# Optimization experiments

Measured on AMD Instinct MI355X. Metric: run time of the kernel, lower is better.

The kernel has to match this reference:

```python
import jax, jax.numpy as jnp
import numpy as np

B, H, L, D, LBL = 512, 64, 528, 32, 10
NI = 64          # number of interval breakpoints
W = 128          # vf MLP width
N_STEPS = 256    # fixed Tsit5 steps over [t0, t1]

# Tsit5 Butcher tableau
C2, C3, C4, C5, C6 = 0.161, 0.327, 0.9, 0.9800255409045097, 1.0
A21 = 0.161
A31, A32 = -0.008480655492356989, 0.335480655492357
A41, A42, A43 = 2.8971530571054935, -6.359448489975075, 4.3622954328695815
A51, A52, A53, A54 = 5.325864828439257, -11.748883564062828, 7.4955393428898365, -0.09249506636175525
A61, A62, A63, A64, A65 = 5.86145544294642, -12.92096931784711, 8.159367898576159, -0.071584973281401, -0.028269050394068383
B1, B2, B3, B4, B5, B6 = 0.09646076681806523, 0.01, 0.4798896504144996, 1.379008574103742, -3.290069515436081, 2.324710524099774


def _linear_init(k, out_dim, in_dim):
    lim = 1.0 / np.sqrt(in_dim)
    kw, kb = jax.random.split(k)
    w = jax.random.uniform(kw, (out_dim, in_dim), jnp.float32, -lim, lim)
    b = jax.random.uniform(kb, (out_dim,), jnp.float32, -lim, lim)
    return w, b


def setup_inputs() -> dict:
    key = jax.random.key(0)
    ks = jax.random.split(key, 8)
    ts = jnp.linspace(0.0, 1.0, 129, dtype=jnp.float32)
    logsig = 0.1 * jax.random.normal(ks[0], (B, NI + 1, L + 1), jnp.float32)
    x0 = jax.random.normal(ks[1], (B, D), jnp.float32)
    intervals = jnp.linspace(0.0, 1.0, NI, dtype=jnp.float32)
    vf_w0, vf_b0 = _linear_init(ks[2], W, H)
    vf_w1, vf_b1 = _linear_init(ks[3], W, W)
    vf_w2, vf_b2 = _linear_init(ks[4], W, W)
    vf_w3, vf_b3 = _linear_init(ks[5], H * L, W)
    l1_w, l1_b = _linear_init(ks[6], H, D)
    l2_w, l2_b = _linear_init(ks[7], LBL, H)
    return dict(ts=ts, logsig=logsig, x0=x0, intervals=intervals,
                vf_w0=vf_w0, vf_b0=vf_b0, vf_w1=vf_w1, vf_b1=vf_b1,
                vf_w2=vf_w2, vf_b2=vf_b2, vf_w3=vf_w3, vf_b3=vf_b3,
                l1_w=l1_w, l1_b=l1_b, l2_w=l2_w, l2_b=l2_b)


def reference(ts, logsig, x0, intervals,
              vf_w0, vf_b0, vf_w1, vf_b1, vf_w2, vf_b2, vf_w3, vf_b3,
              l1_w, l1_b, l2_w, l2_b):
    Bn = x0.shape[0]
    Hn = l1_w.shape[0]
    Ln = vf_b3.shape[0] // Hn

    def vf(y):  # y: (B, H) -> (B, H, L)
        h = jax.nn.silu(y @ vf_w0.T + vf_b0)
        h = jax.nn.silu(h @ vf_w1.T + vf_b1)
        h = jax.nn.silu(h @ vf_w2.T + vf_b2)
        out = jnp.tanh(h @ vf_w3.T + vf_b3)
        return out.reshape(Bn, Hn, Ln)

    def func(t, y):
        idx = jnp.searchsorted(intervals, t)
        sig = logsig[:, idx, 1:]          # (B, L)
        return jnp.einsum('bhl,bl->bh', vf(y), sig)

    t0, t1 = ts[0], ts[-1]
    dt = (t1 - t0) / N_STEPS

    def step(y, i):
        t = t0 + i * dt
        k1 = func(t, y)
        k2 = func(t + C2 * dt, y + dt * (A21 * k1))
        k3 = func(t + C3 * dt, y + dt * (A31 * k1 + A32 * k2))
        k4 = func(t + C4 * dt, y + dt * (A41 * k1 + A42 * k2 + A43 * k3))
        k5 = func(t + C5 * dt, y + dt * (A51 * k1 + A52 * k2 + A53 * k3 + A54 * k4))
        k6 = func(t + C6 * dt, y + dt * (A61 * k1 + A62 * k2 + A63 * k3 + A64 * k4 + A65 * k5))
        y_new = y + dt * (B1 * k1 + B2 * k2 + B3 * k3 + B4 * k4 + B5 * k5 + B6 * k6)
        return y_new, None

    y0 = x0 @ l1_w.T + l1_b
    yT, _ = jax.lax.scan(step, y0, jnp.arange(N_STEPS, dtype=jnp.float32))
    return jax.nn.softmax(yT @ l2_w.T + l2_b, axis=-1)
```

## Files before the change

kernel.cpp:

```cpp
#include <hip/hip_runtime.h>
#include <stdint.h>

#define NBLK 256
#define NTHR 512

typedef __attribute__((ext_vector_type(8))) short short8;
typedef __attribute__((ext_vector_type(4))) float float4_;

#define WS_BAR  0
#define WS_HDNF 16384
#define WS_KF   (16384 + 131072)
#define WS_SGT  (16384 + 131072 + 262144)

#define LOADC(p)    __hip_atomic_load((p),  __ATOMIC_RELAXED, __HIP_MEMORY_SCOPE_SYSTEM)
#define STOREC(p,v) __hip_atomic_store((p), (v), __ATOMIC_RELAXED, __HIP_MEMORY_SCOPE_SYSTEM)

__device__ __forceinline__ unsigned short f2bf(float x) {
  union { float f; unsigned u; } v; v.f = x;
  return (unsigned short)((v.u + 0x7fffu + ((v.u >> 16) & 1u)) >> 16);
}
__device__ __forceinline__ float fast_exp(float x) {
  return __builtin_amdgcn_exp2f(x * 1.4426950408889634f);
}
__device__ __forceinline__ float fast_tanh(float x) {
  float e = __builtin_amdgcn_exp2f(x * 2.8853900817779268f);
  return fmaf(-2.0f, __builtin_amdgcn_rcpf(e + 1.0f), 1.0f);
}
__device__ __forceinline__ float fast_silu(float x) {
  float e = fast_exp(-x);
  return x * __builtin_amdgcn_rcpf(1.0f + e);
}

__device__ __forceinline__ void gridbar(unsigned* bar, int g, unsigned bn) {
  __syncthreads();
  if (threadIdx.x == 0) {
    unsigned* leaf = bar + 32 * (g & 7);
    unsigned* root = bar + 32 * 8;
    unsigned* gen  = bar + 32 * (9 + (g & 7));
    unsigned a = __hip_atomic_fetch_add(leaf, 1u, __ATOMIC_RELAXED, __HIP_MEMORY_SCOPE_SYSTEM);
    if (a == 32u * bn - 1u) {
      unsigned r = __hip_atomic_fetch_add(root, 1u, __ATOMIC_RELAXED, __HIP_MEMORY_SCOPE_SYSTEM);
      if (r == 8u * bn - 1u) {
        #pragma unroll
        for (int j = 0; j < 8; ++j) STOREC(bar + 32 * (9 + j), bn);
      }
    }
    while (LOADC(gen) < bn) __builtin_amdgcn_s_sleep(1);
  }
  __syncthreads();
}

__device__ __forceinline__ void rgbar(unsigned* bar, int h, int Rg, unsigned bn) {
  __syncthreads();
  if (threadIdx.x == 0) {
    unsigned* base = bar + 32 * (32 + Rg * 16);
    unsigned* leaf = base + 32 * (h & 7);
    unsigned* root = base + 32 * 8;
    unsigned* gen  = base + 32 * 9;
    unsigned a = __hip_atomic_fetch_add(leaf, 1u, __ATOMIC_RELAXED, __HIP_MEMORY_SCOPE_SYSTEM);
    if (a == 8u * bn - 1u) {
      unsigned r = __hip_atomic_fetch_add(root, 1u, __ATOMIC_RELAXED, __HIP_MEMORY_SCOPE_SYSTEM);
      if (r == 8u * bn - 1u) STOREC(gen, bn);
    }
    while (LOADC(gen) < bn) __builtin_amdgcn_s_sleep(1);
  }
  __syncthreads();
}

template<int SIN>
__device__ __forceinline__ void rk_stage(
    int stepi, int sg, int g, int h, int Rg, int R,
    float (&kh)[6], float& y, float t0v, float dtv,
    unsigned char* ws, unsigned* BAR, unsigned& gseq, unsigned& rseq, int& last_idx,
    const float* logsig, const float* w0, const float* b0,
    const float* w1, const float* b1, const float* w2, const float* b2,
    unsigned short* w3lds, float* b3lds, float* intv,
    float (*yst)[64], float (*hb1)[128], float (*hb2)[128],
    unsigned short (*hdnS)[128], int* sidxp, int* sidxnp) {
  const int tid = threadIdx.x;
  const int lane = tid & 63, wv = tid >> 6;
  const int col = lane & 15, qd = lane >> 4;
  unsigned* HDNF = (unsigned*)(ws + WS_HDNF);
  float* KF  = (float*)(ws + WS_KF);
  float* SGT = (float*)(ws + WS_SGT);

  if (sg > 0 && tid < 128) {
    const float* KFr = KF + ((sg & 1) ^ 1) * 32768;
    constexpr int pi = (SIN == 0) ? 5 : SIN - 1;
    kh[pi] = LOADC(&KFr[(size_t)(2 * g + (tid >> 6)) * 64 + (tid & 63)]);
  }
  if (tid < 128) {
    float ystv;
    if constexpr (SIN == 0) {
      if (sg > 0) {
        y += dtv * (0.09646076681806523f * kh[0] + 0.01f * kh[1]
                  + 0.4798896504144996f * kh[2] + 1.379008574103742f * kh[3]
                  - 3.290069515436081f * kh[4] + 2.324710524099774f * kh[5]);
      }
      ystv = y;
    } else if constexpr (SIN == 1) {
      ystv = y + dtv * (0.161f * kh[0]);
    } else if constexpr (SIN == 2) {
      ystv = y + dtv * (-0.008480655492356989f * kh[0] + 0.335480655492357f * kh[1]);
    } else if constexpr (SIN == 3) {
      ystv = y + dtv * (2.8971530571054935f * kh[0] - 6.359448489975075f * kh[1]
                      + 4.3622954328695815f * kh[2]);
    } else if constexpr (SIN == 4) {
      ystv = y + dtv * (5.325864828439257f * kh[0] - 11.748883564062828f * kh[1]
                      + 7.4955393428898365f * kh[2] - 0.09249506636175525f * kh[3]);
    } else {
      ystv = y + dtv * (5.86145544294642f * kh[0] - 12.92096931784711f * kh[1]
                      + 8.159367898576159f * kh[2] - 0.071584973281401f * kh[3]
                      - 0.028269050394068383f * kh[4]);
    }
    yst[tid >> 6][tid & 63] = ystv;
  }
  {
    float tb = __fadd_rn(t0v, __fmul_rn((float)stepi, dtv));
    float t_cur, t_nxt;
    if constexpr (SIN == 0) t_cur = tb;
    else {
      constexpr float cS = (SIN == 1) ? 0.161f : (SIN == 2) ? 0.327f : (SIN == 3) ? 0.9f
                         : (SIN == 4) ? 0.9800255409045097f : 1.0f;
      t_cur = __fadd_rn(tb, __fmul_rn(cS, dtv));
    }
    if constexpr (SIN == 5) t_nxt = __fadd_rn(t0v, __fmul_rn((float)(stepi + 1), dtv));
    else {
      constexpr float cN = (SIN == 0) ? 0.161f : (SIN == 1) ? 0.327f : (SIN == 2) ? 0.9f
                         : (SIN == 3) ? 0.9800255409045097f : 1.0f;
      t_nxt = __fadd_rn(tb, __fmul_rn(cN, dtv));
    }
    if (tid < 64) {
      unsigned long long m1 = __ballot(intv[tid] < t_cur);
      unsigned long long m2 = __ballot(intv[tid] < t_nxt);
      if (tid == 0) { *sidxp = (int)__popcll(m1); *sidxnp = (int)__popcll(m2); }
    }
  }
  __syncthreads();
  const int idx = *sidxp, idxn = *sidxnp;
  const bool rebuild = (idx != last_idx);
  const bool rebuild_next = (idxn != idx);
  last_idx = idx;
  if (rebuild && g < 33) {
    const int l0t = g * 16;
    const int part = tid & 3;
    #pragma unroll 1
    for (int bi = 0; bi < 4; ++bi) {
      const int b = bi * 128 + (tid >> 2);
      const float* srow = logsig + ((size_t)b * 65 + idx) * 529 + 1 + l0t + part * 4;
      #pragma unroll
      for (int c2 = 0; c2 < 4; ++c2)
        STOREC(&SGT[(size_t)(l0t + part * 4 + c2) * 512 + b], srow[c2]);
    }
  }
  if (tid < 256) {
    const int row = tid >> 7, j = tid & 127;
    float acc = b0[j];
    const float4_* wr = (const float4_*)(w0 + (size_t)j * 64);
    #pragma unroll
    for (int i4 = 0; i4 < 16; ++i4) {
      float4_ wvv = wr[i4];
      acc = fmaf(yst[row][4*i4+0], wvv[0], acc);
      acc = fmaf(yst[row][4*i4+1], wvv[1], acc);
      acc = fmaf(yst[row][4*i4+2], wvv[2], acc);
      acc = fmaf(yst[row][4*i4+3], wvv[3], acc);
    }
    hb1[row][j] = fast_silu(acc);
  }
  __syncthreads();
  if (tid < 256) {
    const int row = tid >> 7, j = tid & 127;
    float acc = b1[j];
    const float4_* wr = (const float4_*)(w1 + (size_t)j * 128);
    #pragma unroll
    for (int i4 = 0; i4 < 32; ++i4) {
      float4_ wvv = wr[i4];
      acc = fmaf(hb1[row][4*i4+0], wvv[0], acc);
      acc = fmaf(hb1[row][4*i4+1], wvv[1], acc);
      acc = fmaf(hb1[row][4*i4+2], wvv[2], acc);
      acc = fmaf(hb1[row][4*i4+3], wvv[3], acc);
    }
    hb2[row][j] = fast_silu(acc);
  }
  __syncthreads();
  if (tid < 256) {
    const int row = tid >> 7, j = tid & 127;
    float acc = b2[j];
    const float4_* wr = (const float4_*)(w2 + (size_t)j * 128);
    #pragma unroll
    for (int i4 = 0; i4 < 32; ++i4) {
      float4_ wvv = wr[i4];
      acc = fmaf(hb2[row][4*i4+0], wvv[0], acc);
      acc = fmaf(hb2[row][4*i4+1], wvv[1], acc);
      acc = fmaf(hb2[row][4*i4+2], wvv[2], acc);
      acc = fmaf(hb2[row][4*i4+3], wvv[3], acc);
    }
    hdnS[row][j] = f2bf(fast_silu(acc));
  }
  __syncthreads();
  if (tid < 128) {
    const int row = tid >> 6, u = tid & 63;
    const int lb = 2 * h + row;
    const int tile = lb >> 4, colp = lb & 15;
    const int j0 = 2 * u;
    const int kb = j0 >> 5, qdp = (j0 >> 3) & 3, jj = j0 & 7;
    unsigned v = (unsigned)hdnS[row][j0] | ((unsigned)hdnS[row][j0 + 1] << 16);
    unsigned i16 = (unsigned)((Rg * 32 + tile * 4 + kb) * 512 + qdp * 128 + colp * 8 + jj);
    STOREC(&HDNF[i16 >> 1], v);
  }
  if (rebuild) {
    ++gseq; gridbar(BAR, g, gseq);
    __builtin_amdgcn_fence(__ATOMIC_ACQUIRE, "agent");
  } else {
    ++rseq; rgbar(BAR, h, Rg, rseq);
  }

  {
    const unsigned long long* H64 = (const unsigned long long*)HDNF;
    union { unsigned long long u[2]; short8 s; } af[4];
    #pragma unroll
    for (int kb = 0; kb < 4; ++kb) {
      const unsigned i16 = (unsigned)((Rg * 32 + wv * 4 + kb) * 512 + lane * 8);
      af[kb].u[0] = LOADC(&H64[i16 >> 2]);
      af[kb].u[1] = LOADC(&H64[(i16 >> 2) + 1]);
    }
    float kp[4] = {0.0f, 0.0f, 0.0f, 0.0f};
    #pragma unroll 2
    for (int nt = 0; nt < 33; ++nt) {
      const int l = nt * 16 + col;
      const float bv = b3lds[l];
      float4_ acc; acc[0] = bv; acc[1] = bv; acc[2] = bv; acc[3] = bv;
      #pragma unroll
      for (int kb = 0; kb < 4; ++kb) {
        const short8 bf = *(const short8*)(w3lds + ((nt * 4 + kb) * 64 + lane) * 8);
        acc = __builtin_amdgcn_mfma_f32_16x16x32_bf16(af[kb].s, bf, acc, 0, 0, 0);
      }
      const float4_ s4 = *(const float4_*)(SGT + (size_t)l * 512 + R + wv * 16 + qd * 4);
      #pragma unroll
      for (int r = 0; r < 4; ++r)
        kp[r] = fmaf(fast_tanh(acc[r]), s4[r], kp[r]);
    }
    #pragma unroll
    for (int r = 0; r < 4; ++r) {
      float v = kp[r];
      v += __shfl_xor(v, 1); v += __shfl_xor(v, 2);
      v += __shfl_xor(v, 4); v += __shfl_xor(v, 8);
      kp[r] = v;
    }
    if (col == 0) {
      float* KFw = KF + (sg & 1) * 32768;
      #pragma unroll
      for (int r = 0; r < 4; ++r)
        STOREC(&KFw[(size_t)(R + wv * 16 + qd * 4 + r) * 64 + h], kp[r]);
    }
  }
  if (rebuild_next) { ++gseq; gridbar(BAR, g, gseq); }
  else              { ++rseq; rgbar(BAR, h, Rg, rseq); }
}

__global__ void __launch_bounds__(NTHR, 2)
rde_kernel(const float* __restrict__ ts, const float* __restrict__ logsig,
           const float* __restrict__ x0, const float* __restrict__ intervals,
           const float* __restrict__ w0, const float* __restrict__ b0,
           const float* __restrict__ w1, const float* __restrict__ b1,
           const float* __restrict__ w2, const float* __restrict__ b2,
           const float* __restrict__ w3, const float* __restrict__ b3,
           const float* __restrict__ l1w, const float* __restrict__ l1b,
           const float* __restrict__ l2w, const float* __restrict__ l2b,
           float* out, unsigned char* ws) {
  const int tid = threadIdx.x;
  const int g = blockIdx.x;
  const int h = g & 63;
  const int Rg = g >> 6;
  const int R = Rg * 128;
  unsigned* BAR = (unsigned*)(ws + WS_BAR);
  unsigned gseq = 0, rseq = 0;
  int last_idx = -1;

  __shared__ __attribute__((aligned(16))) unsigned short w3lds[67584];
  __shared__ float b3lds[528];
  __shared__ float intv[64];
  __shared__ float yst[2][64];
  __shared__ float hb1[2][128];
  __shared__ float hb2[2][128];
  __shared__ __attribute__((aligned(8))) unsigned short hdnS[2][128];
  __shared__ int sidx, sidxn;

  if (tid < 64) intv[tid] = intervals[tid];
  for (int e = tid; e < 528; e += NTHR) b3lds[e] = b3[(size_t)h * 528 + e];

  for (int e = tid; e < 8448; e += NTHR) {
    const int ln = e & 63, kb = (e >> 6) & 3, nt = e >> 8;
    const float* src = w3 + ((size_t)(h * 528 + nt * 16 + (ln & 15))) * 128 + kb * 32 + (ln >> 4) * 8;
    union { unsigned short s[8]; short8 v; } p;
    #pragma unroll
    for (int j = 0; j < 8; ++j) p.s[j] = f2bf(src[j]);
    *(short8*)(w3lds + e * 8) = p.v;
  }

  float y = 0.0f, kh[6];
  #pragma unroll
  for (int i = 0; i < 6; ++i) kh[i] = 0.0f;
  if (tid < 128) {
    const int row = tid >> 6, hh = tid & 63;
    float acc = l1b[hh];
    const float4_* xr = (const float4_*)(x0 + (size_t)(2 * g + row) * 32);
    const float4_* wr = (const float4_*)(l1w + (size_t)hh * 32);
    #pragma unroll
    for (int d = 0; d < 8; ++d) {
      float4_ xv = xr[d], wvv = wr[d];
      acc = fmaf(xv[0], wvv[0], acc); acc = fmaf(xv[1], wvv[1], acc);
      acc = fmaf(xv[2], wvv[2], acc); acc = fmaf(xv[3], wvv[3], acc);
    }
    y = acc;
  }
  const float t0v = ts[0];
  const float dtv = (ts[128] - t0v) * (1.0f / 256.0f);
  __syncthreads();

  for (int stepi = 0; stepi < 256; ++stepi) {
    const int sg = stepi * 6;
    rk_stage<0>(stepi, sg + 0, g, h, Rg, R, kh, y, t0v, dtv, ws, BAR, gseq, rseq, last_idx,
                logsig, w0, b0, w1, b1, w2, b2, w3lds, b3lds, intv, yst, hb1, hb2, hdnS, &sidx, &sidxn);
    rk_stage<1>(stepi, sg + 1, g, h, Rg, R, kh, y, t0v, dtv, ws, BAR, gseq, rseq, last_idx,
                logsig, w0, b0, w1, b1, w2, b2, w3lds, b3lds, intv, yst, hb1, hb2, hdnS, &sidx, &sidxn);
    rk_stage<2>(stepi, sg + 2, g, h, Rg, R, kh, y, t0v, dtv, ws, BAR, gseq, rseq, last_idx,
                logsig, w0, b0, w1, b1, w2, b2, w3lds, b3lds, intv, yst, hb1, hb2, hdnS, &sidx, &sidxn);
    rk_stage<3>(stepi, sg + 3, g, h, Rg, R, kh, y, t0v, dtv, ws, BAR, gseq, rseq, last_idx,
                logsig, w0, b0, w1, b1, w2, b2, w3lds, b3lds, intv, yst, hb1, hb2, hdnS, &sidx, &sidxn);
    rk_stage<4>(stepi, sg + 4, g, h, Rg, R, kh, y, t0v, dtv, ws, BAR, gseq, rseq, last_idx,
                logsig, w0, b0, w1, b1, w2, b2, w3lds, b3lds, intv, yst, hb1, hb2, hdnS, &sidx, &sidxn);
    rk_stage<5>(stepi, sg + 5, g, h, Rg, R, kh, y, t0v, dtv, ws, BAR, gseq, rseq, last_idx,
                logsig, w0, b0, w1, b1, w2, b2, w3lds, b3lds, intv, yst, hb1, hb2, hdnS, &sidx, &sidxn);
  }

  {
    float* KF = (float*)(ws + WS_KF);
    if (tid < 128) {
      const int row = tid >> 6, hh = tid & 63;
      kh[5] = LOADC(&KF[(size_t)32768 + (size_t)(2 * g + row) * 64 + hh]);
      y += dtv * (0.09646076681806523f * kh[0] + 0.01f * kh[1]
                + 0.4798896504144996f * kh[2] + 1.379008574103742f * kh[3]
                - 3.290069515436081f * kh[4] + 2.324710524099774f * kh[5]);
      yst[row][hh] = y;
    }
    __syncthreads();
    if (tid < 20) {
      const int row = tid / 10, c = tid % 10;
      float acc = l2b[c];
      const float* wr = l2w + c * 64;
      #pragma unroll
      for (int i2 = 0; i2 < 64; ++i2) acc = fmaf(yst[row][i2], wr[i2], acc);
      hb1[row][c] = acc;
    }
    __syncthreads();
    if (tid < 2) {
      const int row = tid;
      float mx = -1e30f;
      for (int c = 0; c < 10; ++c) mx = fmaxf(mx, hb1[row][c]);
      float ev[10], den = 0.0f;
      for (int c = 0; c < 10; ++c) { ev[c] = expf(hb1[row][c] - mx); den += ev[c]; }
      const float rd = 1.0f / den;
      for (int c = 0; c < 10; ++c) out[(size_t)(2 * g + row) * 10 + c] = ev[c] * rd;
    }
  }
}

extern "C" void kernel_launch(void* const* d_in, const int* in_sizes, int n_in,
                              void* d_out, int out_size, void* d_ws, size_t ws_size,
                              hipStream_t stream) {
  (void)in_sizes; (void)n_in; (void)out_size; (void)ws_size;
  const float* ts        = (const float*)d_in[0];
  const float* logsig    = (const float*)d_in[1];
  const float* x0        = (const float*)d_in[2];
  const float* intervals = (const float*)d_in[3];
  const float* w0        = (const float*)d_in[4];
  const float* b0        = (const float*)d_in[5];
  const float* w1        = (const float*)d_in[6];
  const float* b1        = (const float*)d_in[7];
  const float* w2        = (const float*)d_in[8];
  const float* b2        = (const float*)d_in[9];
  const float* w3        = (const float*)d_in[10];
  const float* b3        = (const float*)d_in[11];
  const float* l1w       = (const float*)d_in[12];
  const float* l1b       = (const float*)d_in[13];
  const float* l2w       = (const float*)d_in[14];
  const float* l2b       = (const float*)d_in[15];
  float* out = (float*)d_out;
  unsigned char* ws = (unsigned char*)d_ws;

  hipMemsetAsync(d_ws, 0, 12288, stream);

  void* args[] = { &ts, &logsig, &x0, &intervals, &w0, &b0, &w1, &b1,
                   &w2, &b2, &w3, &b3, &l1w, &l1b, &l2w, &l2b, &out, &ws };
  hipLaunchCooperativeKernel((void*)rde_kernel, dim3(NBLK), dim3(NTHR), args, 0, stream);
}
```

Measured before the change: 38.40 ms.

## Replace tree barriers with per-row-group flag slots and read logsig directly

Removes the grid-wide and tree-structured row-group barriers and replaces them with a flat slot barrier: each block publishes its sequence number and one wavefront polls all 64 peer slots with a ballot. The transposed logsig staging buffer and its grid barriers on interval changes are dropped, and the tanh-weighted reduction now reads logsig rows straight from global memory. The small MLP dot products also split into four partial accumulators to shorten FMA dependency chains. The trade is uncoalesced global reads of logsig on every stage and heavier polling traffic from 64 lanes per block.

```diff
diff --git a/kernel.cpp b/kernel.cpp
--- a/kernel.cpp
+++ b/kernel.cpp
@@ -10,7 +10,6 @@
 #define WS_BAR  0
 #define WS_HDNF 16384
 #define WS_KF   (16384 + 131072)
-#define WS_SGT  (16384 + 131072 + 262144)
 
 #define LOADC(p)    __hip_atomic_load((p),  __ATOMIC_RELAXED, __HIP_MEMORY_SCOPE_SYSTEM)
 #define STOREC(p,v) __hip_atomic_store((p), (v), __ATOMIC_RELAXED, __HIP_MEMORY_SCOPE_SYSTEM)
@@ -31,38 +30,11 @@
   return x * __builtin_amdgcn_rcpf(1.0f + e);
 }
 
-__device__ __forceinline__ void gridbar(unsigned* bar, int g, unsigned bn) {
-  __syncthreads();
-  if (threadIdx.x == 0) {
-    unsigned* leaf = bar + 32 * (g & 7);
-    unsigned* root = bar + 32 * 8;
-    unsigned* gen  = bar + 32 * (9 + (g & 7));
-    unsigned a = __hip_atomic_fetch_add(leaf, 1u, __ATOMIC_RELAXED, __HIP_MEMORY_SCOPE_SYSTEM);
-    if (a == 32u * bn - 1u) {
-      unsigned r = __hip_atomic_fetch_add(root, 1u, __ATOMIC_RELAXED, __HIP_MEMORY_SCOPE_SYSTEM);
-      if (r == 8u * bn - 1u) {
-        #pragma unroll
-        for (int j = 0; j < 8; ++j) STOREC(bar + 32 * (9 + j), bn);
-      }
-    }
-    while (LOADC(gen) < bn) __builtin_amdgcn_s_sleep(1);
-  }
-  __syncthreads();
-}
-
-__device__ __forceinline__ void rgbar(unsigned* bar, int h, int Rg, unsigned bn) {
-  __syncthreads();
-  if (threadIdx.x == 0) {
-    unsigned* base = bar + 32 * (32 + Rg * 16);
-    unsigned* leaf = base + 32 * (h & 7);
-    unsigned* root = base + 32 * 8;
-    unsigned* gen  = base + 32 * 9;
-    unsigned a = __hip_atomic_fetch_add(leaf, 1u, __ATOMIC_RELAXED, __HIP_MEMORY_SCOPE_SYSTEM);
-    if (a == 8u * bn - 1u) {
-      unsigned r = __hip_atomic_fetch_add(root, 1u, __ATOMIC_RELAXED, __HIP_MEMORY_SCOPE_SYSTEM);
-      if (r == 8u * bn - 1u) STOREC(gen, bn);
-    }
-    while (LOADC(gen) < bn) __builtin_amdgcn_s_sleep(1);
+__device__ __forceinline__ void rgbar(unsigned* slots, int h, unsigned seq) {
+  __syncthreads();
+  if (threadIdx.x < 64) {
+    if (threadIdx.x == 0) STOREC(&slots[h], seq);
+    while (__ballot(LOADC(&slots[threadIdx.x]) >= seq) != ~0ull) { }
   }
   __syncthreads();
 }
@@ -71,18 +43,17 @@
 __device__ __forceinline__ void rk_stage(
     int stepi, int sg, int g, int h, int Rg, int R,
     float (&kh)[6], float& y, float t0v, float dtv,
-    unsigned char* ws, unsigned* BAR, unsigned& gseq, unsigned& rseq, int& last_idx,
+    unsigned char* ws, unsigned* slots, unsigned& rseq,
     const float* logsig, const float* w0, const float* b0,
     const float* w1, const float* b1, const float* w2, const float* b2,
     unsigned short* w3lds, float* b3lds, float* intv,
     float (*yst)[64], float (*hb1)[128], float (*hb2)[128],
-    unsigned short (*hdnS)[128], int* sidxp, int* sidxnp) {
+    unsigned short (*hdnS)[128], int* sidxp) {
   const int tid = threadIdx.x;
   const int lane = tid & 63, wv = tid >> 6;
   const int col = lane & 15, qd = lane >> 4;
   unsigned* HDNF = (unsigned*)(ws + WS_HDNF);
   float* KF  = (float*)(ws + WS_KF);
-  float* SGT = (float*)(ws + WS_SGT);
 
   if (sg > 0 && tid < 128) {
     const float* KFr = KF + ((sg & 1) ^ 1) * 32768;
@@ -117,85 +88,64 @@
   }
   {
     float tb = __fadd_rn(t0v, __fmul_rn((float)stepi, dtv));
-    float t_cur, t_nxt;
+    float t_cur;
     if constexpr (SIN == 0) t_cur = tb;
     else {
       constexpr float cS = (SIN == 1) ? 0.161f : (SIN == 2) ? 0.327f : (SIN == 3) ? 0.9f
                          : (SIN == 4) ? 0.9800255409045097f : 1.0f;
       t_cur = __fadd_rn(tb, __fmul_rn(cS, dtv));
     }
-    if constexpr (SIN == 5) t_nxt = __fadd_rn(t0v, __fmul_rn((float)(stepi + 1), dtv));
-    else {
-      constexpr float cN = (SIN == 0) ? 0.161f : (SIN == 1) ? 0.327f : (SIN == 2) ? 0.9f
-                         : (SIN == 3) ? 0.9800255409045097f : 1.0f;
-      t_nxt = __fadd_rn(tb, __fmul_rn(cN, dtv));
-    }
     if (tid < 64) {
       unsigned long long m1 = __ballot(intv[tid] < t_cur);
-      unsigned long long m2 = __ballot(intv[tid] < t_nxt);
-      if (tid == 0) { *sidxp = (int)__popcll(m1); *sidxnp = (int)__popcll(m2); }
-    }
-  }
-  __syncthreads();
-  const int idx = *sidxp, idxn = *sidxnp;
-  const bool rebuild = (idx != last_idx);
-  const bool rebuild_next = (idxn != idx);
-  last_idx = idx;
-  if (rebuild && g < 33) {
-    const int l0t = g * 16;
-    const int part = tid & 3;
-    #pragma unroll 1
-    for (int bi = 0; bi < 4; ++bi) {
-      const int b = bi * 128 + (tid >> 2);
-      const float* srow = logsig + ((size_t)b * 65 + idx) * 529 + 1 + l0t + part * 4;
-      #pragma unroll
-      for (int c2 = 0; c2 < 4; ++c2)
-        STOREC(&SGT[(size_t)(l0t + part * 4 + c2) * 512 + b], srow[c2]);
-    }
-  }
+      if (tid == 0) *sidxp = (int)__popcll(m1);
+    }
+  }
+  __syncthreads();
+  const int idx = *sidxp;
+
   if (tid < 256) {
     const int row = tid >> 7, j = tid & 127;
-    float acc = b0[j];
     const float4_* wr = (const float4_*)(w0 + (size_t)j * 64);
+    float ac[4] = {b0[j], 0.0f, 0.0f, 0.0f};
     #pragma unroll
     for (int i4 = 0; i4 < 16; ++i4) {
       float4_ wvv = wr[i4];
-      acc = fmaf(yst[row][4*i4+0], wvv[0], acc);
-      acc = fmaf(yst[row][4*i4+1], wvv[1], acc);
-      acc = fmaf(yst[row][4*i4+2], wvv[2], acc);
-      acc = fmaf(yst[row][4*i4+3], wvv[3], acc);
-    }
-    hb1[row][j] = fast_silu(acc);
+      float s = fmaf(yst[row][4*i4+0], wvv[0], yst[row][4*i4+1] * wvv[1]);
+      s = fmaf(yst[row][4*i4+2], wvv[2], s);
+      s = fmaf(yst[row][4*i4+3], wvv[3], s);
+      ac[i4 & 3] += s;
+    }
+    hb1[row][j] = fast_silu((ac[0] + ac[1]) + (ac[2] + ac[3]));
   }
   __syncthreads();
   if (tid < 256) {
     const int row = tid >> 7, j = tid & 127;
-    float acc = b1[j];
     const float4_* wr = (const float4_*)(w1 + (size_t)j * 128);
+    float ac[4] = {b1[j], 0.0f, 0.0f, 0.0f};
     #pragma unroll
     for (int i4 = 0; i4 < 32; ++i4) {
       float4_ wvv = wr[i4];
-      acc = fmaf(hb1[row][4*i4+0], wvv[0], acc);
-      acc = fmaf(hb1[row][4*i4+1], wvv[1], acc);
-      acc = fmaf(hb1[row][4*i4+2], wvv[2], acc);
-      acc = fmaf(hb1[row][4*i4+3], wvv[3], acc);
-    }
-    hb2[row][j] = fast_silu(acc);
+      float s = fmaf(hb1[row][4*i4+0], wvv[0], hb1[row][4*i4+1] * wvv[1]);
+      s = fmaf(hb1[row][4*i4+2], wvv[2], s);
+      s = fmaf(hb1[row][4*i4+3], wvv[3], s);
+      ac[i4 & 3] += s;
+    }
+    hb2[row][j] = fast_silu((ac[0] + ac[1]) + (ac[2] + ac[3]));
   }
   __syncthreads();
   if (tid < 256) {
     const int row = tid >> 7, j = tid & 127;
-    float acc = b2[j];
     const float4_* wr = (const float4_*)(w2 + (size_t)j * 128);
+    float ac[4] = {b2[j], 0.0f, 0.0f, 0.0f};
     #pragma unroll
     for (int i4 = 0; i4 < 32; ++i4) {
       float4_ wvv = wr[i4];
-      acc = fmaf(hb2[row][4*i4+0], wvv[0], acc);
-      acc = fmaf(hb2[row][4*i4+1], wvv[1], acc);
-      acc = fmaf(hb2[row][4*i4+2], wvv[2], acc);
-      acc = fmaf(hb2[row][4*i4+3], wvv[3], acc);
-    }
-    hdnS[row][j] = f2bf(fast_silu(acc));
+      float s = fmaf(hb2[row][4*i4+0], wvv[0], hb2[row][4*i4+1] * wvv[1]);
+      s = fmaf(hb2[row][4*i4+2], wvv[2], s);
+      s = fmaf(hb2[row][4*i4+3], wvv[3], s);
+      ac[i4 & 3] += s;
+    }
+    hdnS[row][j] = f2bf(fast_silu((ac[0] + ac[1]) + (ac[2] + ac[3])));
   }
   __syncthreads();
   if (tid < 128) {
@@ -208,12 +158,7 @@
     unsigned i16 = (unsigned)((Rg * 32 + tile * 4 + kb) * 512 + qdp * 128 + colp * 8 + jj);
     STOREC(&HDNF[i16 >> 1], v);
   }
-  if (rebuild) {
-    ++gseq; gridbar(BAR, g, gseq);
-    __builtin_amdgcn_fence(__ATOMIC_ACQUIRE, "agent");
-  } else {
-    ++rseq; rgbar(BAR, h, Rg, rseq);
-  }
+  ++rseq; rgbar(slots, h, rseq);
 
   {
     const unsigned long long* H64 = (const unsigned long long*)HDNF;
@@ -224,6 +169,10 @@
       af[kb].u[0] = LOADC(&H64[i16 >> 2]);
       af[kb].u[1] = LOADC(&H64[(i16 >> 2) + 1]);
     }
+    const float* sp0 = logsig + (size_t)(R + wv * 16 + qd * 4) * 34385 + (size_t)idx * 529 + 1;
+    const float* sp1 = sp0 + 34385;
+    const float* sp2 = sp0 + 2 * 34385;
+    const float* sp3 = sp0 + 3 * 34385;
     float kp[4] = {0.0f, 0.0f, 0.0f, 0.0f};
     #pragma unroll 2
     for (int nt = 0; nt < 33; ++nt) {
@@ -235,10 +184,10 @@
         const short8 bf = *(const short8*)(w3lds + ((nt * 4 + kb) * 64 + lane) * 8);
         acc = __builtin_amdgcn_mfma_f32_16x16x32_bf16(af[kb].s, bf, acc, 0, 0, 0);
       }
-      const float4_ s4 = *(const float4_*)(SGT + (size_t)l * 512 + R + wv * 16 + qd * 4);
-      #pragma unroll
-      for (int r = 0; r < 4; ++r)
-        kp[r] = fmaf(fast_tanh(acc[r]), s4[r], kp[r]);
+      kp[0] = fmaf(fast_tanh(acc[0]), sp0[l], kp[0]);
+      kp[1] = fmaf(fast_tanh(acc[1]), sp1[l], kp[1]);
+      kp[2] = fmaf(fast_tanh(acc[2]), sp2[l], kp[2]);
+      kp[3] = fmaf(fast_tanh(acc[3]), sp3[l], kp[3]);
     }
     #pragma unroll
     for (int r = 0; r < 4; ++r) {
@@ -254,8 +203,7 @@
         STOREC(&KFw[(size_t)(R + wv * 16 + qd * 4 + r) * 64 + h], kp[r]);
     }
   }
-  if (rebuild_next) { ++gseq; gridbar(BAR, g, gseq); }
-  else              { ++rseq; rgbar(BAR, h, Rg, rseq); }
+  ++rseq; rgbar(slots, h, rseq);
 }
 
 __global__ void __launch_bounds__(NTHR, 2)
@@ -273,9 +221,8 @@
   const int h = g & 63;
   const int Rg = g >> 6;
   const int R = Rg * 128;
-  unsigned* BAR = (unsigned*)(ws + WS_BAR);
-  unsigned gseq = 0, rseq = 0;
-  int last_idx = -1;
+  unsigned* slots = (unsigned*)(ws + WS_BAR) + (size_t)Rg * 128;
+  unsigned rseq = 0;
 
   __shared__ __attribute__((aligned(16))) unsigned short w3lds[67584];
   __shared__ float b3lds[528];
@@ -284,7 +231,7 @@
   __shared__ float hb1[2][128];
   __shared__ float hb2[2][128];
   __shared__ __attribute__((aligned(8))) unsigned short hdnS[2][128];
-  __shared__ int sidx, sidxn;
+  __shared__ int sidx;
 
   if (tid < 64) intv[tid] = intervals[tid];
   for (int e = tid; e < 528; e += NTHR) b3lds[e] = b3[(size_t)h * 528 + e];
@@ -320,18 +267,18 @@
 
   for (int stepi = 0; stepi < 256; ++stepi) {
     const int sg = stepi * 6;
-    rk_stage<0>(stepi, sg + 0, g, h, Rg, R, kh, y, t0v, dtv, ws, BAR, gseq, rseq, last_idx,
-                logsig, w0, b0, w1, b1, w2, b2, w3lds, b3lds, intv, yst, hb1, hb2, hdnS, &sidx, &sidxn);
-    rk_stage<1>(stepi, sg + 1, g, h, Rg, R, kh, y, t0v, dtv, ws, BAR, gseq, rseq, last_idx,
-                logsig, w0, b0, w1, b1, w2, b2, w3lds, b3lds, intv, yst, hb1, hb2, hdnS, &sidx, &sidxn);
-    rk_stage<2>(stepi, sg + 2, g, h, Rg, R, kh, y, t0v, dtv, ws, BAR, gseq, rseq, last_idx,
-                logsig, w0, b0, w1, b1, w2, b2, w3lds, b3lds, intv, yst, hb1, hb2, hdnS, &sidx, &sidxn);
-    rk_stage<3>(stepi, sg + 3, g, h, Rg, R, kh, y, t0v, dtv, ws, BAR, gseq, rseq, last_idx,
-                logsig, w0, b0, w1, b1, w2, b2, w3lds, b3lds, intv, yst, hb1, hb2, hdnS, &sidx, &sidxn);
-    rk_stage<4>(stepi, sg + 4, g, h, Rg, R, kh, y, t0v, dtv, ws, BAR, gseq, rseq, last_idx,
-                logsig, w0, b0, w1, b1, w2, b2, w3lds, b3lds, intv, yst, hb1, hb2, hdnS, &sidx, &sidxn);
-    rk_stage<5>(stepi, sg + 5, g, h, Rg, R, kh, y, t0v, dtv, ws, BAR, gseq, rseq, last_idx,
-                logsig, w0, b0, w1, b1, w2, b2, w3lds, b3lds, intv, yst, hb1, hb2, hdnS, &sidx, &sidxn);
+    rk_stage<0>(stepi, sg + 0, g, h, Rg, R, kh, y, t0v, dtv, ws, slots, rseq,
+                logsig, w0, b0, w1, b1, w2, b2, w3lds, b3lds, intv, yst, hb1, hb2, hdnS, &sidx);
+    rk_stage<1>(stepi, sg + 1, g, h, Rg, R, kh, y, t0v, dtv, ws, slots, rseq,
+                logsig, w0, b0, w1, b1, w2, b2, w3lds, b3lds, intv, yst, hb1, hb2, hdnS, &sidx);
+    rk_stage<2>(stepi, sg + 2, g, h, Rg, R, kh, y, t0v, dtv, ws, slots, rseq,
+                logsig, w0, b0, w1, b1, w2, b2, w3lds, b3lds, intv, yst, hb1, hb2, hdnS, &sidx);
+    rk_stage<3>(stepi, sg + 3, g, h, Rg, R, kh, y, t0v, dtv, ws, slots, rseq,
+                logsig, w0, b0, w1, b1, w2, b2, w3lds, b3lds, intv, yst, hb1, hb2, hdnS, &sidx);
+    rk_stage<4>(stepi, sg + 4, g, h, Rg, R, kh, y, t0v, dtv, ws, slots, rseq,
+                logsig, w0, b0, w1, b1, w2, b2, w3lds, b3lds, intv, yst, hb1, hb2, hdnS, &sidx);
+    rk_stage<5>(stepi, sg + 5, g, h, Rg, R, kh, y, t0v, dtv, ws, slots, rseq,
+                logsig, w0, b0, w1, b1, w2, b2, w3lds, b3lds, intv, yst, hb1, hb2, hdnS, &sidx);
   }
 
   {
@@ -389,7 +336,7 @@
   float* out = (float*)d_out;
   unsigned char* ws = (unsigned char*)d_ws;
 
-  hipMemsetAsync(d_ws, 0, 12288, stream);
+  hipMemsetAsync(d_ws, 0, 4096, stream);
 
   void* args[] = { &ts, &logsig, &x0, &intervals, &w0, &b0, &w1, &b1,
                    &w2, &b2, &w3, &b3, &l1w, &l1b, &l2w, &l2b, &out, &ws };
```

After: 46.25 ms. +20.5%, slower.
